# Kernel tuning notes

Hardware: AMD Instinct MI355X
Metric: run time of the kernel (lower is better)

Reference implementation:

```python
import jax, jax.numpy as jnp
import numpy as np
import math

D = 512      # input_size == hidden_size
TAU = 4      # length of att/spatial lists
N = 16384    # tokens (batch*H*W)

def setup_inputs() -> dict:
    key = jax.random.key(0)
    ks = jax.random.split(key, 16)
    s = 1.0 / math.sqrt(D)
    return {
        "T_t": jax.random.normal(ks[0], (N, D), jnp.float32),
        "S_t": jax.random.normal(ks[1], (N, D), jnp.float32),
        "t_att": jax.random.normal(ks[2], (TAU, N, D), jnp.float32),
        "s_att": jax.random.normal(ks[3], (TAU, N, D), jnp.float32),
        "t_spatial": jax.random.normal(ks[4], (TAU, N, D), jnp.float32),
        "s_spatial": jax.random.normal(ks[5], (TAU, N, D), jnp.float32),
        # fl_t: Linear(D, 3D); fl_t_next: Linear(D, D); same for s
        "W_t": jax.random.uniform(ks[6], (3 * D, D), jnp.float32, -s, s),
        "b_t": jax.random.uniform(ks[7], (3 * D,), jnp.float32, -s, s),
        "W_tn": jax.random.uniform(ks[8], (D, D), jnp.float32, -s, s),
        "b_tn": jax.random.uniform(ks[9], (D,), jnp.float32, -s, s),
        "W_s": jax.random.uniform(ks[10], (3 * D, D), jnp.float32, -s, s),
        "b_s": jax.random.uniform(ks[11], (3 * D,), jnp.float32, -s, s),
        "W_sn": jax.random.uniform(ks[12], (D, D), jnp.float32, -s, s),
        "b_sn": jax.random.uniform(ks[13], (D,), jnp.float32, -s, s),
    }

def reference(T_t, S_t, t_att, s_att, t_spatial, s_spatial,
              W_t, b_t, W_tn, b_tn, W_s, b_s, W_sn, b_sn):
    d = T_t.shape[-1]
    scale = 1.0 / jnp.sqrt(jnp.asarray(d, T_t.dtype))
    s_next = S_t @ W_sn.T + b_sn          # [N, D]
    t_next = T_t @ W_tn.T + b_tn          # [N, D]

    # trend weights: dot-product along feature dim, softmax over tau axis
    w_s = jax.nn.softmax(jnp.einsum('knd,nd->kn', s_att, s_next) * scale, axis=0)
    w_t = jax.nn.softmax(jnp.einsum('knd,nd->kn', t_spatial, t_next) * scale, axis=0)
    T_trend = jnp.einsum('knd,kn->nd', t_att, w_s)      # [N, D]
    S_trend = jnp.einsum('knd,kn->nd', s_spatial, w_t)  # [N, D]

    t_gate = jax.nn.sigmoid(t_next)
    s_gate = jax.nn.sigmoid(s_next)
    T_fusion = T_t * t_gate + (1.0 - t_gate) * T_trend
    S_fusion = S_t * s_gate + (1.0 - s_gate) * S_trend

    T_concat = T_fusion @ W_t.T + b_t     # [N, 3D]
    S_concat = S_fusion @ W_s.T + b_s
    t_g, t_t, t_s = jnp.split(T_concat, 3, axis=1)
    s_g, s_t, s_s = jnp.split(S_concat, 3, axis=1)
    T_gate = jax.nn.sigmoid(t_g)
    S_gate = jax.nn.sigmoid(s_g)
    T_new = T_gate * t_t + (1.0 - T_gate) * s_t
    S_new = S_gate * s_s + (1.0 - S_gate) * t_s
    return T_new, S_new
```

## Files before the change

### kernel.cpp

```cpp
#include <hip/hip_runtime.h>

#define NTOK 16384
#define DIM 512
#define NTAU 4

typedef __attribute__((ext_vector_type(4))) float f32x4;
typedef __attribute__((ext_vector_type(8))) short bf16x8;
typedef __attribute__((ext_vector_type(4))) unsigned short u16x4;
typedef __attribute__((ext_vector_type(8))) unsigned short u16x8;
typedef unsigned int u32;

__device__ inline unsigned short f2bf(float f) {
    union { float f; unsigned int u; } v; v.f = f;
    unsigned int u = v.u + 0x7FFFu + ((v.u >> 16) & 1u);
    return (unsigned short)(u >> 16);
}

__device__ inline void bf8_to_f32(u16x8 h, f32x4& a, f32x4& b) {
    union { unsigned int u; float f; } t;
#pragma unroll
    for (int e = 0; e < 4; e++) { t.u = ((unsigned int)h[e]) << 16; a[e] = t.f; }
#pragma unroll
    for (int e = 0; e < 4; e++) { t.u = ((unsigned int)h[4 + e]) << 16; b[e] = t.f; }
}

#define NTLOAD4(p) __builtin_nontemporal_load((const f32x4*)(p))

__device__ __forceinline__ void gload16(const void* g, void* l) {
    __builtin_amdgcn_global_load_lds((const __attribute__((address_space(1))) u32*)g,
                                     (__attribute__((address_space(3))) u32*)l, 16, 0, 0);
}

__global__ void convert_all(const float* __restrict__ a, const float* __restrict__ b,
                            const float* __restrict__ c, const float* __restrict__ d,
                            unsigned short* __restrict__ oa, unsigned short* __restrict__ ob,
                            unsigned short* __restrict__ oc, unsigned short* __restrict__ od) {
    int i = blockIdx.x * 256 + threadIdx.x;
    const float* s; unsigned short* t; int off;
    if (i < 65536)       { s = a; t = oa; off = i; }
    else if (i < 131072) { s = b; t = ob; off = i - 65536; }
    else if (i < 327680) { s = c; t = oc; off = i - 131072; }
    else                 { s = d; t = od; off = i - 327680; }
    f32x4 v = ((const f32x4*)s)[off];
    u16x4 o;
    o[0] = f2bf(v[0]); o[1] = f2bf(v[1]); o[2] = f2bf(v[2]); o[3] = f2bf(v[3]);
    ((u16x4*)t)[off] = o;
}

__global__ __launch_bounds__(256, 2) void gemm_next2(
    const float* __restrict__ T_t, const float* __restrict__ S_t,
    const unsigned short* __restrict__ Wtn, const unsigned short* __restrict__ Wsn,
    const float* __restrict__ btn, const float* __restrict__ bsn,
    unsigned short* __restrict__ t_next, unsigned short* __restrict__ s_next)
{
    __shared__ unsigned short lA[128][40];
    __shared__ unsigned short lB[128][40];
    const int tid = threadIdx.x;
    const int id = blockIdx.x;
    const int xcd = id & 7;
    const int rest = id >> 3;
    const int mat = rest & 1;
    const int idx = rest >> 1;
    const float* A = mat ? S_t : T_t;
    const unsigned short* W = mat ? Wsn : Wtn;
    const float* bias = mat ? bsn : btn;
    unsigned short* out = mat ? s_next : t_next;
    const int m0 = (xcd * 16 + (idx >> 2)) * 128;
    const int n0 = (idx & 3) * 128;
    const int lane = tid & 63;
    const int w = tid >> 6;
    const int wr = w >> 1, wc = w & 1;

    f32x4 acc[4][4];
#pragma unroll
    for (int i = 0; i < 4; i++)
#pragma unroll
        for (int j = 0; j < 4; j++) acc[i][j] = (f32x4){0.f, 0.f, 0.f, 0.f};

    const int arow = tid >> 3;
    const int acol = (tid & 7) * 4;
    const int brow = tid >> 2;
    const int bcol = (tid & 3) * 8;

    for (int k0 = 0; k0 < DIM; k0 += 32) {
#pragma unroll
        for (int i = 0; i < 4; i++) {
            int r = arow + 32 * i;
            f32x4 v = *(const f32x4*)(A + (size_t)(m0 + r) * DIM + k0 + acol);
            u16x4 o;
            o[0] = f2bf(v[0]); o[1] = f2bf(v[1]); o[2] = f2bf(v[2]); o[3] = f2bf(v[3]);
            *(u16x4*)&lA[r][acol] = o;
        }
#pragma unroll
        for (int i = 0; i < 2; i++) {
            int r = brow + 64 * i;
            u16x8 v = *(const u16x8*)(W + (size_t)(n0 + r) * DIM + k0 + bcol);
            *(u16x8*)&lB[r][bcol] = v;
        }
        __syncthreads();

        bf16x8 af[4], bfr[4];
#pragma unroll
        for (int i = 0; i < 4; i++)
            af[i] = *(const bf16x8*)&lA[wr * 64 + i * 16 + (lane & 15)][(lane >> 4) * 8];
#pragma unroll
        for (int j = 0; j < 4; j++)
            bfr[j] = *(const bf16x8*)&lB[wc * 64 + j * 16 + (lane & 15)][(lane >> 4) * 8];
#pragma unroll
        for (int i = 0; i < 4; i++)
#pragma unroll
            for (int j = 0; j < 4; j++)
                acc[i][j] = __builtin_amdgcn_mfma_f32_16x16x32_bf16(af[i], bfr[j], acc[i][j], 0, 0, 0);
        __syncthreads();
    }

#pragma unroll
    for (int j = 0; j < 4; j++) {
        int n = n0 + wc * 64 + j * 16 + (lane & 15);
        float bv = bias[n];
#pragma unroll
        for (int i = 0; i < 4; i++) {
            int mbase = m0 + wr * 64 + i * 16 + (lane >> 4) * 4;
#pragma unroll
            for (int r = 0; r < 4; r++)
                out[(size_t)(mbase + r) * DIM + n] = f2bf(acc[i][j][r] + bv);
        }
    }
}

__global__ __launch_bounds__(256) void dots_kernel(
    const float* __restrict__ s_att, const float* __restrict__ t_spatial,
    const unsigned short* __restrict__ t_next, const unsigned short* __restrict__ s_next,
    float* __restrict__ w_all)
{
    const int lane = threadIdx.x & 63;
    const int id = blockIdx.x;
    const int n = (id & 7) * 2048 + (id >> 3) * 4 + (threadIdx.x >> 6);
    const int c = lane * 8;
    const size_t rb = (size_t)n * DIM + c;
    const float scale = 0.04419417382415922f;

    f32x4 tn_a, tn_b, sn_a, sn_b;
    bf8_to_f32(*(const u16x8*)(t_next + rb), tn_a, tn_b);
    bf8_to_f32(*(const u16x8*)(s_next + rb), sn_a, sn_b);

    float dws[NTAU], dwt[NTAU];
#pragma unroll
    for (int k = 0; k < NTAU; k++) {
        const size_t kb = ((size_t)k * NTOK + n) * DIM + c;
        f32x4 a0 = NTLOAD4(s_att + kb);
        f32x4 a1 = NTLOAD4(s_att + kb + 4);
        f32x4 b0 = NTLOAD4(t_spatial + kb);
        f32x4 b1 = NTLOAD4(t_spatial + kb + 4);
        dws[k] = a0[0]*sn_a[0]+a0[1]*sn_a[1]+a0[2]*sn_a[2]+a0[3]*sn_a[3]
               + a1[0]*sn_b[0]+a1[1]*sn_b[1]+a1[2]*sn_b[2]+a1[3]*sn_b[3];
        dwt[k] = b0[0]*tn_a[0]+b0[1]*tn_a[1]+b0[2]*tn_a[2]+b0[3]*tn_a[3]
               + b1[0]*tn_b[0]+b1[1]*tn_b[1]+b1[2]*tn_b[2]+b1[3]*tn_b[3];
    }
#pragma unroll
    for (int k = 0; k < NTAU; k++) {
        float v = dws[k];
#pragma unroll
        for (int off = 32; off; off >>= 1) v += __shfl_xor(v, off);
        dws[k] = v * scale;
        float u = dwt[k];
#pragma unroll
        for (int off = 32; off; off >>= 1) u += __shfl_xor(u, off);
        dwt[k] = u * scale;
    }

    float ms = fmaxf(fmaxf(dws[0], dws[1]), fmaxf(dws[2], dws[3]));
    float mt = fmaxf(fmaxf(dwt[0], dwt[1]), fmaxf(dwt[2], dwt[3]));
    f32x4 wsv, wtv;
    float ssum = 0.f, tsum = 0.f;
#pragma unroll
    for (int k = 0; k < NTAU; k++) {
        wsv[k] = __expf(dws[k] - ms); ssum += wsv[k];
        wtv[k] = __expf(dwt[k] - mt); tsum += wtv[k];
    }
    float rs = 1.f / ssum, rt = 1.f / tsum;
#pragma unroll
    for (int k = 0; k < NTAU; k++) { wsv[k] *= rs; wtv[k] *= rt; }

    if (lane == 0) {
        *(f32x4*)(w_all + (size_t)n * 8)     = wsv;
        *(f32x4*)(w_all + (size_t)n * 8 + 4) = wtv;
    }
}

__global__ __launch_bounds__(256) void fusion_kernel(
    const float* __restrict__ T_t, const float* __restrict__ S_t,
    const float* __restrict__ t_att, const float* __restrict__ s_spatial,
    const unsigned short* __restrict__ t_next, const unsigned short* __restrict__ s_next,
    const float* __restrict__ w_all,
    unsigned short* __restrict__ Tf, unsigned short* __restrict__ Sf)
{
    const int lane = threadIdx.x & 63;
    const int id = blockIdx.x;
    const int n = (id & 7) * 2048 + (id >> 3) * 4 + (threadIdx.x >> 6);
    const int c = lane * 8;
    const size_t rb = (size_t)n * DIM + c;

    f32x4 wsv = *(const f32x4*)(w_all + (size_t)n * 8);
    f32x4 wtv = *(const f32x4*)(w_all + (size_t)n * 8 + 4);

    f32x4 Tta = {0,0,0,0}, Ttb = {0,0,0,0}, Sta = {0,0,0,0}, Stb = {0,0,0,0};
#pragma unroll
    for (int k = 0; k < NTAU; k++) {
        const size_t kb = ((size_t)k * NTOK + n) * DIM + c;
        f32x4 ta = NTLOAD4(t_att + kb);
        f32x4 tb = NTLOAD4(t_att + kb + 4);
        f32x4 sa = NTLOAD4(s_spatial + kb);
        f32x4 sb = NTLOAD4(s_spatial + kb + 4);
        float wk = wsv[k], vk = wtv[k];
#pragma unroll
        for (int e = 0; e < 4; e++) {
            Tta[e] += wk * ta[e]; Ttb[e] += wk * tb[e];
            Sta[e] += vk * sa[e]; Stb[e] += vk * sb[e];
        }
    }

    f32x4 tn_a, tn_b, sn_a, sn_b;
    bf8_to_f32(*(const u16x8*)(t_next + rb), tn_a, tn_b);
    bf8_to_f32(*(const u16x8*)(s_next + rb), sn_a, sn_b);
    f32x4 Ta = NTLOAD4(T_t + rb);
    f32x4 Tb = NTLOAD4(T_t + rb + 4);
    f32x4 Sa = NTLOAD4(S_t + rb);
    f32x4 Sb = NTLOAD4(S_t + rb + 4);

    u16x8 oT, oS;
#pragma unroll
    for (int e = 0; e < 4; e++) {
        float gt_a = 1.f / (1.f + __expf(-tn_a[e]));
        float gt_b = 1.f / (1.f + __expf(-tn_b[e]));
        float gs_a = 1.f / (1.f + __expf(-sn_a[e]));
        float gs_b = 1.f / (1.f + __expf(-sn_b[e]));
        oT[e]     = f2bf(Ta[e] * gt_a + (1.f - gt_a) * Tta[e]);
        oT[4 + e] = f2bf(Tb[e] * gt_b + (1.f - gt_b) * Ttb[e]);
        oS[e]     = f2bf(Sa[e] * gs_a + (1.f - gs_a) * Sta[e]);
        oS[4 + e] = f2bf(Sb[e] * gs_b + (1.f - gs_b) * Stb[e]);
    }
    *(u16x8*)(Tf + rb) = oT;
    *(u16x8*)(Sf + rb) = oS;
}

__global__ __launch_bounds__(256, 2) void gemm_final(
    const unsigned short* __restrict__ Tf, const unsigned short* __restrict__ Sf,
    const unsigned short* __restrict__ Wt, const unsigned short* __restrict__ Ws,
    const float* __restrict__ bt, const float* __restrict__ bs,
    float* __restrict__ out)
{
    __shared__ __align__(16) unsigned char smem[57344];
    auto lT = (unsigned short (*)[128][32])(smem);
    auto lS = (unsigned short (*)[128][32])(smem + 16384);
    auto lW = (unsigned short (*)[192][32])(smem + 32768);
    auto ex = (float (*)[16][132])(smem);

    const int tid = threadIdx.x;
    const int id = blockIdx.x;
    const int xcd = id & 7;
    const int idx = id >> 3;
    const int m0 = (xcd * 16 + (idx >> 4)) * 128;
    const int j0 = (idx & 15) * 32;
    const int lane = tid & 63;
    const int w = tid >> 6;
    const int side = w >> 1;
    const int jq = w & 1;

    f32x4 acc[3][8];
#pragma unroll
    for (int g = 0; g < 3; g++)
#pragma unroll
        for (int i = 0; i < 8; i++) acc[g][i] = (f32x4){0.f, 0.f, 0.f, 0.f};

    const int srow = lane >> 2;
    const int sg   = lane & 3;

    auto stage = [&](int buf, int kt) {
        const int k0 = kt * 32;
#pragma unroll
        for (int i = 0; i < 7; i++) {
            const int ch = w * 7 + i;
            if (ch < 8) {
                const int row = ch * 16 + srow;
                const int lg = sg ^ ((row >> 1) & 3);
                gload16(Tf + (size_t)(m0 + row) * DIM + k0 + lg * 8, &lT[buf][ch * 16][0]);
            } else if (ch < 16) {
                const int row = (ch - 8) * 16 + srow;
                const int lg = sg ^ ((row >> 1) & 3);
                gload16(Sf + (size_t)(m0 + row) * DIM + k0 + lg * 8, &lS[buf][(ch - 8) * 16][0]);
            } else {
                const int rbse = (ch - 16) * 16;
                const int r = rbse + srow;
                const int lg = sg ^ ((r >> 1) & 3);
                const int g = r >> 5;
                const unsigned short* src = (g < 3) ? Wt : Ws;
                const int wrow = (g < 3 ? g : g - 3) * DIM + j0 + (r & 31);
                gload16(src + (size_t)wrow * DIM + k0 + lg * 8, &lW[buf][rbse][0]);
            }
        }
    };

    stage(0, 0);
    __syncthreads();

    int cur = 0;
    for (int kt = 0; kt < 16; ++kt) {
        if (kt < 15) stage(cur ^ 1, kt + 1);

        unsigned short (*lA)[32] = side ? lS[cur] : lT[cur];
        bf16x8 ax[8], bw[3];
#pragma unroll
        for (int i = 0; i < 8; i++) {
            const int row = i * 16 + (lane & 15);
            const int pg = (lane >> 4) ^ ((row >> 1) & 3);
            ax[i] = *(const bf16x8*)&lA[row][pg * 8];
        }
#pragma unroll
        for (int g = 0; g < 3; g++) {
            const int r = (side * 3 + g) * 32 + jq * 16 + (lane & 15);
            const int pg = (lane >> 4) ^ ((r >> 1) & 3);
            bw[g] = *(const bf16x8*)&lW[cur][r][pg * 8];
        }
#pragma unroll
        for (int g = 0; g < 3; g++)
#pragma unroll
            for (int i = 0; i < 8; i++)
                acc[g][i] = __builtin_amdgcn_mfma_f32_16x16x32_bf16(ax[i], bw[g], acc[g][i], 0, 0, 0);

        __syncthreads();
        cur ^= 1;
    }

    const int j = j0 + jq * 16 + (lane & 15);
    const float b0 = side ? bs[j]        : bt[j];
    const float b1 = side ? bs[512 + j]  : bt[512 + j];
    const float b2 = side ? bs[1024 + j] : bt[1024 + j];

    const int col = lane & 15;
#pragma unroll
    for (int i = 0; i < 8; i++) {
        const int rowb = i * 16 + (lane >> 4) * 4;
        f32x4 v = side ? acc[1][i] : acc[2][i];
        const float bb = side ? b1 : b2;
        v[0] += bb; v[1] += bb; v[2] += bb; v[3] += bb;
        *(f32x4*)&ex[w][col][rowb] = v;
    }
    __syncthreads();

    float* obase = out + (side ? (size_t)NTOK * DIM : 0);
    const float bown = side ? b2 : b1;
    const int gown = side ? 2 : 1;
#pragma unroll
    for (int i = 0; i < 8; i++) {
        const int rowb = i * 16 + (lane >> 4) * 4;
        f32x4 oth = *(const f32x4*)&ex[w ^ 2][col][rowb];
#pragma unroll
        for (int r = 0; r < 4; r++) {
            const float gate = 1.f / (1.f + __expf(-(acc[0][i][r] + b0)));
            const float own = acc[gown][i][r] + bown;
            obase[(size_t)(m0 + rowb + r) * DIM + j] = gate * own + (1.f - gate) * oth[r];
        }
    }
}

extern "C" void kernel_launch(void* const* d_in, const int* in_sizes, int n_in,
                              void* d_out, int out_size, void* d_ws, size_t ws_size,
                              hipStream_t stream) {
    const float* T_t       = (const float*)d_in[0];
    const float* S_t       = (const float*)d_in[1];
    const float* t_att     = (const float*)d_in[2];
    const float* s_att     = (const float*)d_in[3];
    const float* t_spatial = (const float*)d_in[4];
    const float* s_spatial = (const float*)d_in[5];
    const float* W_t  = (const float*)d_in[6];
    const float* b_t  = (const float*)d_in[7];
    const float* W_tn = (const float*)d_in[8];
    const float* b_tn = (const float*)d_in[9];
    const float* W_s  = (const float*)d_in[10];
    const float* b_s  = (const float*)d_in[11];
    const float* W_sn = (const float*)d_in[12];
    const float* b_sn = (const float*)d_in[13];
    float* out = (float*)d_out;

    char* ws = (char*)d_ws;
    unsigned short* t_next = (unsigned short*)(ws + 0);
    unsigned short* s_next = (unsigned short*)(ws + 16777216);
    unsigned short* Tf     = (unsigned short*)(ws + 33554432);
    unsigned short* Sf     = (unsigned short*)(ws + 50331648);
    unsigned short* Wtn_b  = (unsigned short*)(ws + 67108864);
    unsigned short* Wsn_b  = (unsigned short*)(ws + 67633152);
    unsigned short* Wt_b   = (unsigned short*)(ws + 68157440);
    unsigned short* Ws_b   = (unsigned short*)(ws + 69730304);
    float*          w_all  = (float*)(ws + 71303168);

    convert_all<<<2048, 256, 0, stream>>>(W_tn, W_sn, W_t, W_s,
                                          Wtn_b, Wsn_b, Wt_b, Ws_b);

    gemm_next2<<<1024, 256, 0, stream>>>(T_t, S_t, Wtn_b, Wsn_b, b_tn, b_sn,
                                         t_next, s_next);

    dots_kernel<<<4096, 256, 0, stream>>>(s_att, t_spatial, t_next, s_next, w_all);

    fusion_kernel<<<4096, 256, 0, stream>>>(T_t, S_t, t_att, s_spatial,
                                            t_next, s_next, w_all, Tf, Sf);

    gemm_final<<<2048, 256, 0, stream>>>(Tf, Sf, Wt_b, Ws_b, b_t, b_s, out);
}
```

Baseline: 290.4 us.

## Split gemm_final across 8 waves with precomputed staging pointers and LDS offsets

The final GEMM block grows from 256 to 512 threads, so each wave now computes half of the 128-row tile (4 MFMA row tiles instead of 8). Global source pointers and LDS read offsets are computed once and advanced each k-step instead of being recomputed in the loop. The aim is more waves to hide latency and lower per-wave register pressure. The cost is more LDS reads per MFMA, because the B fragments are loaded by twice as many waves, plus a changed exchange layout in the epilogue.

```diff
diff --git a/kernel.cpp b/kernel.cpp
--- a/kernel.cpp
+++ b/kernel.cpp
@@ -244,18 +244,13 @@
     *(u16x8*)(Sf + rb) = oS;
 }
 
-__global__ __launch_bounds__(256, 2) void gemm_final(
+__global__ __launch_bounds__(512, 2) void gemm_final(
     const unsigned short* __restrict__ Tf, const unsigned short* __restrict__ Sf,
     const unsigned short* __restrict__ Wt, const unsigned short* __restrict__ Ws,
     const float* __restrict__ bt, const float* __restrict__ bs,
     float* __restrict__ out)
 {
     __shared__ __align__(16) unsigned char smem[57344];
-    auto lT = (unsigned short (*)[128][32])(smem);
-    auto lS = (unsigned short (*)[128][32])(smem + 16384);
-    auto lW = (unsigned short (*)[192][32])(smem + 32768);
-    auto ex = (float (*)[16][132])(smem);
-
     const int tid = threadIdx.x;
     const int id = blockIdx.x;
     const int xcd = id & 7;
@@ -264,68 +259,88 @@
     const int j0 = (idx & 15) * 32;
     const int lane = tid & 63;
     const int w = tid >> 6;
-    const int side = w >> 1;
+    const int side = w >> 2;
+    const int mh = (w >> 1) & 1;
     const int jq = w & 1;
 
-    f32x4 acc[3][8];
+    f32x4 acc[3][4];
 #pragma unroll
     for (int g = 0; g < 3; g++)
 #pragma unroll
-        for (int i = 0; i < 8; i++) acc[g][i] = (f32x4){0.f, 0.f, 0.f, 0.f};
+        for (int i = 0; i < 4; i++) acc[g][i] = (f32x4){0.f, 0.f, 0.f, 0.f};
 
     const int srow = lane >> 2;
     const int sg   = lane & 3;
 
-    auto stage = [&](int buf, int kt) {
-        const int k0 = kt * 32;
-#pragma unroll
-        for (int i = 0; i < 7; i++) {
-            const int ch = w * 7 + i;
-            if (ch < 8) {
-                const int row = ch * 16 + srow;
-                const int lg = sg ^ ((row >> 1) & 3);
-                gload16(Tf + (size_t)(m0 + row) * DIM + k0 + lg * 8, &lT[buf][ch * 16][0]);
-            } else if (ch < 16) {
-                const int row = (ch - 8) * 16 + srow;
-                const int lg = sg ^ ((row >> 1) & 3);
-                gload16(Sf + (size_t)(m0 + row) * DIM + k0 + lg * 8, &lS[buf][(ch - 8) * 16][0]);
-            } else {
-                const int rbse = (ch - 16) * 16;
-                const int r = rbse + srow;
-                const int lg = sg ^ ((r >> 1) & 3);
-                const int g = r >> 5;
-                const unsigned short* src = (g < 3) ? Wt : Ws;
-                const int wrow = (g < 3 ? g : g - 3) * DIM + j0 + (r & 31);
-                gload16(src + (size_t)wrow * DIM + k0 + lg * 8, &lW[buf][rbse][0]);
-            }
+    const unsigned short* gp[4];
+    int nvalid[4];
+#pragma unroll
+    for (int i = 0; i < 4; i++) {
+        const int ch = i * 8 + w;
+        nvalid[i] = (ch < 28);
+        const unsigned short* p = Tf;
+        if (ch < 8) {
+            const int trow = ch * 16 + srow;
+            const int lg = sg ^ ((trow >> 1) & 3);
+            p = Tf + (size_t)(m0 + trow) * DIM + lg * 8;
+        } else if (ch < 16) {
+            const int trow = (ch - 8) * 16 + srow;
+            const int lg = sg ^ ((trow >> 1) & 3);
+            p = Sf + (size_t)(m0 + trow) * DIM + lg * 8;
+        } else if (ch < 28) {
+            const int r = (ch - 16) * 16 + srow;
+            const int lg = sg ^ ((r >> 1) & 3);
+            const int g = r >> 5;
+            const unsigned short* src = (g < 3) ? Wt : Ws;
+            const int wrow = (g < 3 ? g : g - 3) * DIM + j0 + (r & 31);
+            p = src + (size_t)wrow * DIM + lg * 8;
+        }
+        gp[i] = p;
+    }
+
+    int axo[4], bwo[3];
+#pragma unroll
+    for (int i = 0; i < 4; i++) {
+        const int row = mh * 64 + i * 16 + (lane & 15);
+        const int pg = (lane >> 4) ^ ((row >> 1) & 3);
+        axo[i] = ((side * 128 + row) * 32 + pg * 8) * 2;
+    }
+#pragma unroll
+    for (int g = 0; g < 3; g++) {
+        const int r = (side * 3 + g) * 32 + jq * 16 + (lane & 15);
+        const int pg = (lane >> 4) ^ ((r >> 1) & 3);
+        bwo[g] = ((256 + r) * 32 + pg * 8) * 2;
+    }
+
+    auto stage = [&](int buf) {
+#pragma unroll
+        for (int i = 0; i < 4; i++) {
+            if (nvalid[i])
+                gload16(gp[i], smem + buf * 28672 + (i * 8 + w) * 1024);
         }
     };
 
-    stage(0, 0);
+    stage(0);
     __syncthreads();
 
     int cur = 0;
     for (int kt = 0; kt < 16; ++kt) {
-        if (kt < 15) stage(cur ^ 1, kt + 1);
-
-        unsigned short (*lA)[32] = side ? lS[cur] : lT[cur];
-        bf16x8 ax[8], bw[3];
-#pragma unroll
-        for (int i = 0; i < 8; i++) {
-            const int row = i * 16 + (lane & 15);
-            const int pg = (lane >> 4) ^ ((row >> 1) & 3);
-            ax[i] = *(const bf16x8*)&lA[row][pg * 8];
-        }
-#pragma unroll
-        for (int g = 0; g < 3; g++) {
-            const int r = (side * 3 + g) * 32 + jq * 16 + (lane & 15);
-            const int pg = (lane >> 4) ^ ((r >> 1) & 3);
-            bw[g] = *(const bf16x8*)&lW[cur][r][pg * 8];
-        }
+        if (kt < 15) {
+#pragma unroll
+            for (int i = 0; i < 4; i++) gp[i] += 32;
+            stage(cur ^ 1);
+        }
+
+        const unsigned char* base = smem + cur * 28672;
+        bf16x8 ax[4], bw[3];
+#pragma unroll
+        for (int i = 0; i < 4; i++) ax[i] = *(const bf16x8*)(base + axo[i]);
+#pragma unroll
+        for (int g = 0; g < 3; g++) bw[g] = *(const bf16x8*)(base + bwo[g]);
 #pragma unroll
         for (int g = 0; g < 3; g++)
 #pragma unroll
-            for (int i = 0; i < 8; i++)
+            for (int i = 0; i < 4; i++)
                 acc[g][i] = __builtin_amdgcn_mfma_f32_16x16x32_bf16(ax[i], bw[g], acc[g][i], 0, 0, 0);
 
         __syncthreads();
@@ -337,29 +352,31 @@
     const float b1 = side ? bs[512 + j]  : bt[512 + j];
     const float b2 = side ? bs[1024 + j] : bt[1024 + j];
 
+    float* exbase = (float*)smem;
     const int col = lane & 15;
 #pragma unroll
-    for (int i = 0; i < 8; i++) {
+    for (int i = 0; i < 4; i++) {
         const int rowb = i * 16 + (lane >> 4) * 4;
         f32x4 v = side ? acc[1][i] : acc[2][i];
         const float bb = side ? b1 : b2;
         v[0] += bb; v[1] += bb; v[2] += bb; v[3] += bb;
-        *(f32x4*)&ex[w][col][rowb] = v;
+        *(f32x4*)(exbase + ((w * 16 + col) * 68) + rowb) = v;
     }
     __syncthreads();
 
     float* obase = out + (side ? (size_t)NTOK * DIM : 0);
     const float bown = side ? b2 : b1;
-    const int gown = side ? 2 : 1;
-#pragma unroll
-    for (int i = 0; i < 8; i++) {
+    const int pw = w ^ 4;
+#pragma unroll
+    for (int i = 0; i < 4; i++) {
         const int rowb = i * 16 + (lane >> 4) * 4;
-        f32x4 oth = *(const f32x4*)&ex[w ^ 2][col][rowb];
+        f32x4 oth = *(const f32x4*)(exbase + ((pw * 16 + col) * 68) + rowb);
+        f32x4 own = side ? acc[2][i] : acc[1][i];
 #pragma unroll
         for (int r = 0; r < 4; r++) {
             const float gate = 1.f / (1.f + __expf(-(acc[0][i][r] + b0)));
-            const float own = acc[gown][i][r] + bown;
-            obase[(size_t)(m0 + rowb + r) * DIM + j] = gate * own + (1.f - gate) * oth[r];
+            const float ov = own[r] + bown;
+            obase[(size_t)(m0 + mh * 64 + rowb + r) * DIM + j] = gate * ov + (1.f - gate) * oth[r];
         }
     }
 }
@@ -405,5 +422,5 @@
     fusion_kernel<<<4096, 256, 0, stream>>>(T_t, S_t, t_att, s_spatial,
                                             t_next, s_next, w_all, Tf, Sf);
 
-    gemm_final<<<2048, 256, 0, stream>>>(Tf, Sf, Wt_b, Ws_b, b_t, b_s, out);
-}
+    gemm_final<<<2048, 512, 0, stream>>>(Tf, Sf, Wt_b, Ws_b, b_t, b_s, out);
+}
```

Measured after the change: 280.0 us. 3.5% less time.
